# Kernel tuning notes

Measured on AMD Instinct MI355X. Metric: run time of the kernel, lower is better.

Reference implementation:

```python
import jax, jax.numpy as jnp
import numpy as np

LAMBDA_COORD = 5.0
LAMBDA_NOOBJ = 0.5
EPS = 1e-9


def _bbox_iou(px, py, pr, gx, gy, gr):
    """IoU of the axis-aligned bounding squares of two circles (x, y, r)."""
    l1, r1, t1, b1 = px - pr, px + pr, py - pr, py + pr
    l2, r2, t2, b2 = gx - gr, gx + gr, gy - gr, gy + gr
    iw = jnp.maximum(jnp.minimum(r1, r2) - jnp.maximum(l1, l2), 0.0)
    ih = jnp.maximum(jnp.minimum(b1, b2) - jnp.maximum(t1, t2), 0.0)
    inter = iw * ih
    a1 = (r1 - l1) * (b1 - t1)
    a2 = (r2 - l2) * (b2 - t2)
    return inter / (a1 + a2 - inter + EPS)


def setup_inputs() -> dict:
    key = jax.random.key(0)
    k1, k2, k3, k4 = jax.random.split(key, 4)
    B, L, G, C = 65536, 16, 8, 8
    pred = jax.random.uniform(k1, (B, G, G, C), dtype=jnp.float32)
    label_rc = jax.random.randint(k2, (B, L, 2), 0, G, dtype=jnp.int32)
    xy = jax.random.uniform(k3, (B, L, 2), dtype=jnp.float32)
    r = jax.random.uniform(k4, (B, L, 1), dtype=jnp.float32) * 0.2 + 0.01
    label_box = jnp.concatenate([xy, r], axis=-1)
    return {"pred": pred, "label_rc": label_rc, "label_box": label_box}


def reference(pred, label_rc, label_box):
    B = pred.shape[0]
    rows = label_rc[..., 0]  # [B, L]
    cols = label_rc[..., 1]
    bidx = jnp.arange(B)[:, None]
    pb = pred[bidx, rows, cols]  # [B, L, 8] responsible cell per label

    gx, gy, gr = label_box[..., 0], label_box[..., 1], label_box[..., 2]
    iou1 = _bbox_iou(pb[..., 0], pb[..., 1], pb[..., 2], gx, gy, gr)
    iou2 = _bbox_iou(pb[..., 4], pb[..., 5], pb[..., 6], gx, gy, gr)

    swap = iou2 > iou1
    cx = jnp.where(swap, pb[..., 4], pb[..., 0])
    cy = jnp.where(swap, pb[..., 5], pb[..., 1])
    cr = jnp.where(swap, pb[..., 6], pb[..., 2])
    conf = jnp.where(swap, pb[..., 7], pb[..., 3])
    un_conf = jnp.where(swap, pb[..., 3], pb[..., 7])
    bigger = jnp.where(swap, iou2, iou1)
    smaller = jnp.where(swap, iou1, iou2)

    coord_loss = LAMBDA_COORD * jnp.sum(
        (cx - gx) ** 2 + (cy - gy) ** 2 + (cr - gr) ** 2)
    cond_loss = jnp.sum((bigger - conf) ** 2)
    cond_loss = cond_loss + LAMBDA_NOOBJ * jnp.sum((smaller - un_conf) ** 2)

    # object mask over the 8x8 grid (duplicates collapse to 1, as in original)
    obj_mask = jnp.zeros(pred.shape[:3], dtype=pred.dtype).at[bidx, rows, cols].set(1.0)
    noobj = (pred[..., 3] ** 2 + pred[..., 7] ** 2) * (1.0 - obj_mask)
    cond_loss = cond_loss + LAMBDA_NOOBJ * jnp.sum(noobj)

    return (coord_loss + cond_loss) / B
```

## Files before the change

### kernel.cpp

```cpp
#include <hip/hip_runtime.h>


static constexpr float LAMBDA_COORD = 5.0f;
static constexpr float LAMBDA_NOOBJ = 0.5f;
static constexpr float EPS_F = 1e-9f;

#define WAVES_PER_BLOCK  4
#define BATCHES_PER_WAVE 8

__device__ __forceinline__ float bbox_iou(float px, float py, float pr,
                                          float gx, float gy, float gr) {
    float l1 = px - pr, r1 = px + pr, t1 = py - pr, b1 = py + pr;
    float l2 = gx - gr, r2 = gx + gr, t2 = gy - gr, b2 = gy + gr;
    float iw = fmaxf(fminf(r1, r2) - fmaxf(l1, l2), 0.0f);
    float ih = fmaxf(fminf(b1, b2) - fmaxf(t1, t2), 0.0f);
    float inter = iw * ih;
    float a1 = (r1 - l1) * (b1 - t1);
    float a2 = (r2 - l2) * (b2 - t2);
    return inter / (a1 + a2 - inter + EPS_F);
}

__global__ __launch_bounds__(256, 4) void yolo_loss_kernel(
    const float* __restrict__ pred,
    const int*   __restrict__ label_rc,
    const float* __restrict__ label_box,
    float* __restrict__ partials,
    int B, int L)
{
    const int tid  = threadIdx.x;
    const int lane = tid & 63;
    const int wv   = tid >> 6;

    const long wg      = (long)blockIdx.x * WAVES_PER_BLOCK + wv;
    const long b_begin = wg * BATCHES_PER_WAVE;
    long       b_end   = b_begin + BATCHES_PER_WAVE;
    if (b_end > (long)B) b_end = (long)B;

    const bool has_label = (lane < L);
    float acc = 0.0f;

    float4 v0, v1;
    if (b_begin < b_end) {
        const float4* gp = (const float4*)(pred + b_begin * 512);
        v0 = gp[lane];
        v1 = gp[lane + 64];
    }

    for (long b = b_begin; b < b_end; ++b) {
        const float4 c0 = v0, c1 = v1;
        if (b + 1 < b_end) {
            const float4* gp = (const float4*)(pred + (b + 1) * 512);
            v0 = gp[lane];
            v1 = gp[lane + 64];
        }

        int   cell = 0;
        float gx = 0.f, gy = 0.f, gr = 0.f;
        if (has_label) {
            const int2 rc = *(const int2*)(label_rc + ((size_t)b * L + lane) * 2);
            cell = rc.x * 8 + rc.y;
            const float* lb = label_box + ((size_t)b * L + lane) * 3;
            gx = lb[0]; gy = lb[1]; gr = lb[2];
        }

        acc += LAMBDA_NOOBJ * (c0.w * c0.w + c1.w * c1.w);

        const int  q  = cell * 2;
        const bool lo = (q < 64);
        const int  sA = q & 63;
        const int  sB = sA + 1;

        float p0, p1, p2, p3, p4, p5, p6, p7;
        {
            float a, bb;
            a = __shfl(c0.x, sA); bb = __shfl(c1.x, sA); p0 = lo ? a : bb;
            a = __shfl(c0.y, sA); bb = __shfl(c1.y, sA); p1 = lo ? a : bb;
            a = __shfl(c0.z, sA); bb = __shfl(c1.z, sA); p2 = lo ? a : bb;
            a = __shfl(c0.w, sA); bb = __shfl(c1.w, sA); p3 = lo ? a : bb;
            a = __shfl(c0.x, sB); bb = __shfl(c1.x, sB); p4 = lo ? a : bb;
            a = __shfl(c0.y, sB); bb = __shfl(c1.y, sB); p5 = lo ? a : bb;
            a = __shfl(c0.z, sB); bb = __shfl(c1.z, sB); p6 = lo ? a : bb;
            a = __shfl(c0.w, sB); bb = __shfl(c1.w, sB); p7 = lo ? a : bb;
        }

        bool owner = has_label;
        for (int j = 0; j < L; ++j) {
            const int cj = __shfl(cell, j);
            if (j < lane && cj == cell) owner = false;
        }

        if (has_label) {
            const float iou1 = bbox_iou(p0, p1, p2, gx, gy, gr);
            const float iou2 = bbox_iou(p4, p5, p6, gx, gy, gr);
            const bool  sw   = iou2 > iou1;
            const float cx      = sw ? p4 : p0;
            const float cy      = sw ? p5 : p1;
            const float cr      = sw ? p6 : p2;
            const float conf    = sw ? p7 : p3;
            const float un_conf = sw ? p3 : p7;
            const float bigger  = sw ? iou2 : iou1;
            const float smaller = sw ? iou1 : iou2;
            const float dx = cx - gx, dy = cy - gy, dr = cr - gr;
            acc += LAMBDA_COORD * (dx * dx + dy * dy + dr * dr);
            const float d1 = bigger - conf;
            const float d2 = smaller - un_conf;
            acc += d1 * d1 + LAMBDA_NOOBJ * (d2 * d2);
            if (owner)
                acc -= LAMBDA_NOOBJ * (p3 * p3 + p7 * p7);
        }
    }

    #pragma unroll
    for (int off = 32; off > 0; off >>= 1)
        acc += __shfl_xor(acc, off);

    __shared__ float wsum[WAVES_PER_BLOCK];
    if (lane == 0) wsum[wv] = acc;
    __syncthreads();
    if (tid == 0)
        partials[blockIdx.x] = wsum[0] + wsum[1] + wsum[2] + wsum[3];
}

__global__ __launch_bounds__(256) void reduce_kernel(
    const float* __restrict__ partials, float* __restrict__ out,
    int n, float invB)
{
    float s = 0.0f;
    for (int i = threadIdx.x; i < n; i += 256)
        s += partials[i];
    #pragma unroll
    for (int off = 32; off > 0; off >>= 1)
        s += __shfl_xor(s, off);

    __shared__ float wsum[4];
    const int lane = threadIdx.x & 63, w = threadIdx.x >> 6;
    if (lane == 0) wsum[w] = s;
    __syncthreads();
    if (threadIdx.x == 0)
        out[0] = (wsum[0] + wsum[1] + wsum[2] + wsum[3]) * invB;
}

extern "C" void kernel_launch(void* const* d_in, const int* in_sizes, int n_in,
                              void* d_out, int out_size, void* d_ws, size_t ws_size,
                              hipStream_t stream) {
    const float* pred      = (const float*)d_in[0];
    const int*   label_rc  = (const int*)d_in[1];
    const float* label_box = (const float*)d_in[2];
    float*       out       = (float*)d_out;
    float*       partials  = (float*)d_ws;

    const int B = in_sizes[0] / 512;
    const int L = in_sizes[1] / (B * 2);
    const float invB = 1.0f / (float)B;

    const int batches_per_block = WAVES_PER_BLOCK * BATCHES_PER_WAVE;
    const int blocks = (B + batches_per_block - 1) / batches_per_block;

    yolo_loss_kernel<<<blocks, 256, 0, stream>>>(
        pred, label_rc, label_box, partials, B, L);

    reduce_kernel<<<1, 256, 0, stream>>>(partials, out, blocks, invB);
}
```

Measured before the change: 221.4 us.

## Stage pred tiles in LDS and process four batches per wave concurrently

Replaces the per-batch cross-lane shuffle gather with LDS staging. Each wave loads four batches at once, issuing all global loads up front for two super-groups, and writes them to shared memory. Each 16-lane group then handles one batch's labels by indexing the staged cell directly. Duplicate-cell detection moves from a 16-iteration shuffle loop to an LDS atomicOr bitmask. This cuts shuffle instruction count and uses all 64 lanes instead of 16, at the cost of LDS traffic, more registers for the larger prefetch buffers, and reliance on an explicit lgkmcnt wait rather than a barrier, which assumes L ≤ 16.

Result: faster. 206.3 us (-6.8%).

```diff
diff --git a/kernel.cpp b/kernel.cpp
--- a/kernel.cpp
+++ b/kernel.cpp
@@ -5,8 +5,9 @@
 static constexpr float LAMBDA_NOOBJ = 0.5f;
 static constexpr float EPS_F = 1e-9f;
 
-#define WAVES_PER_BLOCK  4
-#define BATCHES_PER_WAVE 8
+#define WAVES_PER_BLOCK 4
+#define SUPER  4
+#define SUPERS 2
 
 __device__ __forceinline__ float bbox_iou(float px, float py, float pr,
                                           float gx, float gy, float gr) {
@@ -20,6 +21,69 @@
     return inter / (a1 + a2 - inter + EPS_F);
 }
 
+#define LOAD_SUPER(dst, b0)                                                    \
+    {                                                                          \
+        _Pragma("unroll")                                                      \
+        for (int q = 0; q < SUPER; ++q) {                                      \
+            const long b_ = (b0) + q;                                          \
+            if (b_ < (long)B) {                                                \
+                const float4* gp_ = (const float4*)(pred + b_ * 512);          \
+                dst[2 * q]     = gp_[lane];                                    \
+                dst[2 * q + 1] = gp_[lane + 64];                               \
+            } else {                                                           \
+                dst[2 * q]     = make_float4(0.f, 0.f, 0.f, 0.f);              \
+                dst[2 * q + 1] = make_float4(0.f, 0.f, 0.f, 0.f);              \
+            }                                                                  \
+        }                                                                      \
+    }
+
+#define PROC_SUPER(buf, b0)                                                    \
+    {                                                                          \
+                            \
+        if (lane < SUPER * 2) my_mask[lane] = 0u;                              \
+        _Pragma("unroll")                                                      \
+        for (int q = 0; q < SUPER; ++q) {                                      \
+            noobj_acc += buf[2 * q].w     * buf[2 * q].w                       \
+                       + buf[2 * q + 1].w * buf[2 * q + 1].w;                  \
+            float4* sp4_ = (float4*)(my_stage + q * 512);                      \
+            sp4_[lane]      = buf[2 * q];                                      \
+            sp4_[lane + 64] = buf[2 * q + 1];                                  \
+        }                                                                      \
+        asm volatile("s_waitcnt lgkmcnt(0)" ::: "memory");                     \
+        const long bq_ = (b0) + grp;                                           \
+        if (bq_ < (long)B && lj < L) {                                         \
+            const int2 rc_ = *(const int2*)(label_rc + ((size_t)bq_ * L + lj) * 2); \
+            const float* lb_ = label_box + ((size_t)bq_ * L + lj) * 3;         \
+            const float gx = lb_[0], gy = lb_[1], gr = lb_[2];                 \
+            const int cell_ = rc_.x * 8 + rc_.y;                               \
+            const float4* cp_ = (const float4*)(my_stage + grp * 512 + cell_ * 8); \
+            const float4 c0_ = cp_[0];                                         \
+            const float4 c1_ = cp_[1];                                         \
+            const unsigned bit_ = 1u << (cell_ & 31);                          \
+            const unsigned old_ = atomicOr(&my_mask[grp * 2 + (cell_ >> 5)], bit_); \
+            const float p0 = c0_.x, p1 = c0_.y, p2 = c0_.z, p3 = c0_.w;        \
+            const float p4 = c1_.x, p5 = c1_.y, p6 = c1_.z, p7 = c1_.w;        \
+            const float iou1 = bbox_iou(p0, p1, p2, gx, gy, gr);               \
+            const float iou2 = bbox_iou(p4, p5, p6, gx, gy, gr);               \
+            const bool  sw_ = iou2 > iou1;                                     \
+            const float cx = sw_ ? p4 : p0;                                    \
+            const float cy = sw_ ? p5 : p1;                                    \
+            const float cr = sw_ ? p6 : p2;                                    \
+            const float conf    = sw_ ? p7 : p3;                               \
+            const float un_conf = sw_ ? p3 : p7;                               \
+            const float bigger  = sw_ ? iou2 : iou1;                           \
+            const float smaller = sw_ ? iou1 : iou2;                           \
+            const float dx = cx - gx, dy = cy - gy, dr = cr - gr;              \
+            main_acc += LAMBDA_COORD * (dx * dx + dy * dy + dr * dr);          \
+            const float d1 = bigger - conf;                                    \
+            main_acc += d1 * d1;                                               \
+            const float d2 = smaller - un_conf;                                \
+            noobj_acc += d2 * d2;                                              \
+            if ((old_ & bit_) == 0u)         \
+                noobj_acc -= (p3 * p3 + p7 * p7);                              \
+        }                                                                      \
+    }
+
 __global__ __launch_bounds__(256, 4) void yolo_loss_kernel(
     const float* __restrict__ pred,
     const int*   __restrict__ label_rc,
@@ -27,94 +91,37 @@
     float* __restrict__ partials,
     int B, int L)
 {
+    __shared__ float    stage[WAVES_PER_BLOCK][SUPER * 512];
+    __shared__ unsigned cmask[WAVES_PER_BLOCK][SUPER * 2];
+    __shared__ float    wsum[WAVES_PER_BLOCK];
+
     const int tid  = threadIdx.x;
     const int lane = tid & 63;
     const int wv   = tid >> 6;
+    const int grp  = lane >> 4;
+    const int lj   = lane & 15;
 
-    const long wg      = (long)blockIdx.x * WAVES_PER_BLOCK + wv;
-    const long b_begin = wg * BATCHES_PER_WAVE;
-    long       b_end   = b_begin + BATCHES_PER_WAVE;
-    if (b_end > (long)B) b_end = (long)B;
+    float*    my_stage = stage[wv];
+    unsigned* my_mask  = cmask[wv];
 
-    const bool has_label = (lane < L);
-    float acc = 0.0f;
+    const long b_base =
+        ((long)blockIdx.x * WAVES_PER_BLOCK + wv) * (SUPER * SUPERS);
 
-    float4 v0, v1;
-    if (b_begin < b_end) {
-        const float4* gp = (const float4*)(pred + b_begin * 512);
-        v0 = gp[lane];
-        v1 = gp[lane + 64];
-    }
+    float main_acc  = 0.0f;
+    float noobj_acc = 0.0f;
 
-    for (long b = b_begin; b < b_end; ++b) {
-        const float4 c0 = v0, c1 = v1;
-        if (b + 1 < b_end) {
-            const float4* gp = (const float4*)(pred + (b + 1) * 512);
-            v0 = gp[lane];
-            v1 = gp[lane + 64];
-        }
+    float4 bufA[2 * SUPER];
+    float4 bufB[2 * SUPER];
+    LOAD_SUPER(bufA, b_base);
+    LOAD_SUPER(bufB, b_base + SUPER);
 
-        int   cell = 0;
-        float gx = 0.f, gy = 0.f, gr = 0.f;
-        if (has_label) {
-            const int2 rc = *(const int2*)(label_rc + ((size_t)b * L + lane) * 2);
-            cell = rc.x * 8 + rc.y;
-            const float* lb = label_box + ((size_t)b * L + lane) * 3;
-            gx = lb[0]; gy = lb[1]; gr = lb[2];
-        }
+    PROC_SUPER(bufA, b_base);
+    PROC_SUPER(bufB, b_base + SUPER);
 
-        acc += LAMBDA_NOOBJ * (c0.w * c0.w + c1.w * c1.w);
-
-        const int  q  = cell * 2;
-        const bool lo = (q < 64);
-        const int  sA = q & 63;
-        const int  sB = sA + 1;
-
-        float p0, p1, p2, p3, p4, p5, p6, p7;
-        {
-            float a, bb;
-            a = __shfl(c0.x, sA); bb = __shfl(c1.x, sA); p0 = lo ? a : bb;
-            a = __shfl(c0.y, sA); bb = __shfl(c1.y, sA); p1 = lo ? a : bb;
-            a = __shfl(c0.z, sA); bb = __shfl(c1.z, sA); p2 = lo ? a : bb;
-            a = __shfl(c0.w, sA); bb = __shfl(c1.w, sA); p3 = lo ? a : bb;
-            a = __shfl(c0.x, sB); bb = __shfl(c1.x, sB); p4 = lo ? a : bb;
-            a = __shfl(c0.y, sB); bb = __shfl(c1.y, sB); p5 = lo ? a : bb;
-            a = __shfl(c0.z, sB); bb = __shfl(c1.z, sB); p6 = lo ? a : bb;
-            a = __shfl(c0.w, sB); bb = __shfl(c1.w, sB); p7 = lo ? a : bb;
-        }
-
-        bool owner = has_label;
-        for (int j = 0; j < L; ++j) {
-            const int cj = __shfl(cell, j);
-            if (j < lane && cj == cell) owner = false;
-        }
-
-        if (has_label) {
-            const float iou1 = bbox_iou(p0, p1, p2, gx, gy, gr);
-            const float iou2 = bbox_iou(p4, p5, p6, gx, gy, gr);
-            const bool  sw   = iou2 > iou1;
-            const float cx      = sw ? p4 : p0;
-            const float cy      = sw ? p5 : p1;
-            const float cr      = sw ? p6 : p2;
-            const float conf    = sw ? p7 : p3;
-            const float un_conf = sw ? p3 : p7;
-            const float bigger  = sw ? iou2 : iou1;
-            const float smaller = sw ? iou1 : iou2;
-            const float dx = cx - gx, dy = cy - gy, dr = cr - gr;
-            acc += LAMBDA_COORD * (dx * dx + dy * dy + dr * dr);
-            const float d1 = bigger - conf;
-            const float d2 = smaller - un_conf;
-            acc += d1 * d1 + LAMBDA_NOOBJ * (d2 * d2);
-            if (owner)
-                acc -= LAMBDA_NOOBJ * (p3 * p3 + p7 * p7);
-        }
-    }
-
+    float acc = main_acc + LAMBDA_NOOBJ * noobj_acc;
     #pragma unroll
     for (int off = 32; off > 0; off >>= 1)
         acc += __shfl_xor(acc, off);
-
-    __shared__ float wsum[WAVES_PER_BLOCK];
     if (lane == 0) wsum[wv] = acc;
     __syncthreads();
     if (tid == 0)
@@ -153,7 +160,7 @@
     const int L = in_sizes[1] / (B * 2);
     const float invB = 1.0f / (float)B;
 
-    const int batches_per_block = WAVES_PER_BLOCK * BATCHES_PER_WAVE;
+    const int batches_per_block = WAVES_PER_BLOCK * SUPER * SUPERS;
     const int blocks = (B + batches_per_block - 1) / batches_per_block;
 
     yolo_loss_kernel<<<blocks, 256, 0, stream>>>(
```
